# Kernel optimization log

Measured on AMD Instinct MI355X. Metric: run time of the kernel, lower is better.

## Reference

```python
import jax, jax.numpy as jnp
import numpy as np

B = 2; QD = 128; H = QD; W = QD; NQ = QD * QD
EMBED = 256; HEADS = 8; POINTS = 4; D = EMBED // HEADS; FFN = 512


def setup_inputs() -> dict:
    key = jax.random.key(0)
    ks = jax.random.split(key, 16)
    s = 0.02
    rn = lambda k, shp: jax.random.normal(k, shp, jnp.float32) * s
    return {
        'q': jax.random.normal(ks[0], (B, NQ, EMBED), jnp.float32),
        'W_off': rn(ks[1], (EMBED, HEADS * POINTS * 2)),
        'b_off': rn(ks[2], (HEADS * POINTS * 2,)),
        'W_attn': rn(ks[3], (EMBED, HEADS * POINTS)),
        'b_attn': rn(ks[4], (HEADS * POINTS,)),
        'W_val': rn(ks[5], (EMBED, EMBED)),
        'b_val': rn(ks[6], (EMBED,)),
        'W_out': rn(ks[7], (EMBED, EMBED)),
        'b_out': rn(ks[8], (EMBED,)),
        'W1': rn(ks[9], (EMBED, FFN)),
        'b1': rn(ks[10], (FFN,)),
        'W2': rn(ks[11], (FFN, EMBED)),
        'b2': rn(ks[12], (EMBED,)),
        'gamma': jnp.ones((EMBED,), jnp.float32),
        'beta': jnp.zeros((EMBED,), jnp.float32),
    }


def _layernorm(x, g, b):
    m = x.mean(-1, keepdims=True)
    v = ((x - m) ** 2).mean(-1, keepdims=True)
    return (x - m) * jax.lax.rsqrt(v + 1e-5) * g + b


def _msda(q, W_off, b_off, W_attn, b_attn, W_val, b_val, W_out, b_out):
    # value projection; value == query here. (B, NQ, EMBED)
    value = q @ W_val + b_val
    v = value.reshape(B, NQ, HEADS, D).transpose(0, 2, 1, 3)  # (B, heads, Nv, D)

    off = (q @ W_off + b_off).reshape(B, NQ, HEADS, POINTS, 2)
    aw = jax.nn.softmax((q @ W_attn + b_attn).reshape(B, NQ, HEADS, POINTS), axis=-1)

    # reference points: torch.meshgrid(linspace, linspace, indexing='xy')
    lin = jnp.linspace(0.0, 1.0, QD)
    gx, gy = jnp.meshgrid(lin, lin, indexing='xy')
    ref = jnp.stack([gx, gy], -1).reshape(1, NQ, 1, 1, 2)

    # offset_normalizer = [W, H]; sampling locations in [0,1]
    loc = ref + off / jnp.array([W, H], jnp.float32)
    # grid_sample bilinear, align_corners=False: pixel = loc * size - 0.5
    px = (loc[..., 0] * W - 0.5).transpose(0, 2, 1, 3)  # (B, heads, NQ, P)
    py = (loc[..., 1] * H - 0.5).transpose(0, 2, 1, 3)

    x0 = jnp.floor(px)
    y0 = jnp.floor(py)
    sampled = jnp.zeros((B, HEADS, NQ, POINTS, D), jnp.float32)
    for dy in (0.0, 1.0):
        for dx in (0.0, 1.0):
            xi = x0 + dx
            yi = y0 + dy
            wgt = (1.0 - jnp.abs(px - xi)) * (1.0 - jnp.abs(py - yi))
            valid = ((xi >= 0) & (xi <= W - 1) & (yi >= 0) & (yi <= H - 1)).astype(jnp.float32)
            idx = (jnp.clip(yi, 0, H - 1).astype(jnp.int32) * W
                   + jnp.clip(xi, 0, W - 1).astype(jnp.int32))  # (B, heads, NQ, P)
            g = jnp.take_along_axis(v, idx.reshape(B, HEADS, NQ * POINTS, 1), axis=2)
            g = g.reshape(B, HEADS, NQ, POINTS, D)
            sampled = sampled + g * (wgt * valid)[..., None]

    awt = aw.transpose(0, 2, 1, 3)  # (B, heads, NQ, P)
    out = (sampled * awt[..., None]).sum(3)  # (B, heads, NQ, D)
    out = out.transpose(0, 2, 1, 3).reshape(B, NQ, EMBED)
    # mmcv: dropout(output_proj(out)) + identity ; dropout is identity at eval
    return out @ W_out + b_out + q


def reference(q, W_off, b_off, W_attn, b_attn, W_val, b_val, W_out, b_out,
              W1, b1, W2, b2, gamma, beta):
    attn = _msda(q, W_off, b_off, W_attn, b_attn, W_val, b_val, W_out, b_out)
    x = attn + q  # outer residual in the module (in addition to mmcv's internal one)
    ffn = _layernorm(jax.nn.relu(x @ W1 + b1) @ W2 + b2, gamma, beta)
    return x + ffn
```

## Files before the change

kernel.cpp:

```cpp
#include <hip/hip_runtime.h>
#include <hip/hip_bf16.h>
#include <cstddef>
#include <cstdint>

#define B_      2
#define QD_     128
#define NQ_     (QD_ * QD_)
#define EMBED_  256
#define HEADS_  8
#define POINTS_ 4
#define FFN_    512
#define RTOT_   (B_ * NQ_)
#define NCATP_  384

using bf16x8 = __attribute__((ext_vector_type(8))) short;
using f32x4  = __attribute__((ext_vector_type(4))) float;

__device__ __forceinline__ short f2bf(float f) {
    unsigned u = __float_as_uint(f);
    u += 0x7FFFu + ((u >> 16) & 1u);
    return (short)(u >> 16);
}

#define WCAT_ELEMS  (NCATP_ * 256)
#define WOUT_ELEMS  (256 * 256)
#define W1_ELEMS    (512 * 256)
#define W2_ELEMS    (256 * 512)
#define PREP_TOTAL  (WCAT_ELEMS + WOUT_ELEMS + W1_ELEMS + W2_ELEMS)

__global__ __launch_bounds__(256) void prep_weights(
        const float* __restrict__ Wv, const float* __restrict__ Wo,
        const float* __restrict__ Wa, const float* __restrict__ bv,
        const float* __restrict__ bo, const float* __restrict__ ba,
        const float* __restrict__ W_out, const float* __restrict__ W1,
        const float* __restrict__ W2,
        short* __restrict__ WcatT, short* __restrict__ WoutT,
        short* __restrict__ W1T, short* __restrict__ W2T,
        float* __restrict__ bcat) {
    int idx = blockIdx.x * 256 + threadIdx.x;
    if (idx < WCAT_ELEMS) {
        int c = idx >> 8, k = idx & 255;
        float v = 0.f;
        if (c < 256)      v = Wv[k * 256 + c];
        else if (c < 320) v = Wo[k * 64 + (c - 256)];
        else if (c < 352) v = Wa[k * 32 + (c - 320)];
        WcatT[idx] = f2bf(v);
    } else if (idx < WCAT_ELEMS + WOUT_ELEMS) {
        int j = idx - WCAT_ELEMS; int c = j >> 8, k = j & 255;
        WoutT[j] = f2bf(W_out[k * 256 + c]);
    } else if (idx < WCAT_ELEMS + WOUT_ELEMS + W1_ELEMS) {
        int j = idx - (WCAT_ELEMS + WOUT_ELEMS); int c = j >> 8, k = j & 255;
        W1T[j] = f2bf(W1[k * 512 + c]);
    } else if (idx < PREP_TOTAL) {
        int j = idx - (WCAT_ELEMS + WOUT_ELEMS + W1_ELEMS); int c = j >> 9, k = j & 511;
        W2T[j] = f2bf(W2[k * 256 + c]);
    }
    if (idx < NCATP_) {
        float v = 0.f;
        if (idx < 256)      v = bv[idx];
        else if (idx < 320) v = bo[idx - 256];
        else if (idx < 352) v = ba[idx - 320];
        bcat[idx] = v;
    }
}

__global__ __launch_bounds__(256) void cvt_bf16(const float* __restrict__ in,
                                                short* __restrict__ out) {
    const size_t i = (size_t)blockIdx.x * 256 + threadIdx.x;
    const float4 f0 = *(const float4*)(in + i * 8);
    const float4 f1 = *(const float4*)(in + i * 8 + 4);
    bf16x8 v;
    v[0] = f2bf(f0.x); v[1] = f2bf(f0.y); v[2] = f2bf(f0.z); v[3] = f2bf(f0.w);
    v[4] = f2bf(f1.x); v[5] = f2bf(f1.y); v[6] = f2bf(f1.z); v[7] = f2bf(f1.w);
    *(bf16x8*)(out + i * 8) = v;
}

enum { EP_F32 = 0, EP_RELU_BF16 = 1, EP_ADD2Q_BOTH = 2, EP_SPLIT = 3 };

template <int EP>
__global__ __launch_bounds__(256) void gemm_mfma(
        const short* __restrict__ A,
        const short* __restrict__ Bt,
        const float* __restrict__ bias,
        const float* __restrict__ extra,
        float* __restrict__ Cf,
        short* __restrict__ Cb,
        int M, int N, int K) {
    __shared__ __align__(16) short As[128 * 64];
    __shared__ __align__(16) short Bs[128 * 64];

    const int t    = threadIdx.x;
    const int ln   = t & 63;
    const int w    = t >> 6;
    const int wr   = w >> 1;
    const int wc   = w & 1;
    const int lrow = ln & 15;
    const int lkg  = ln >> 4;
    const int row0 = blockIdx.y * 128;
    const int col0 = blockIdx.x * 128;

    f32x4 acc[4][4] = {};

    for (int k0 = 0; k0 < K; k0 += 64) {
        #pragma unroll
        for (int j = 0; j < 4; ++j) {
            const int c0 = (w * 4 + j) * 64;
            const int c  = c0 + ln;
            const int r  = c >> 3;
            const int s  = (c & 7) ^ (r & 7);
            const short* ga = A  + (size_t)(row0 + r) * K + (k0 + s * 8);
            const short* gb = Bt + (size_t)(col0 + r) * K + (k0 + s * 8);
            __builtin_amdgcn_global_load_lds(
                (const __attribute__((address_space(1))) void*)ga,
                (__attribute__((address_space(3))) void*)&As[c0 * 8], 16, 0, 0);
            __builtin_amdgcn_global_load_lds(
                (const __attribute__((address_space(1))) void*)gb,
                (__attribute__((address_space(3))) void*)&Bs[c0 * 8], 16, 0, 0);
        }
        __syncthreads();

        #pragma unroll
        for (int ks = 0; ks < 2; ++ks) {
            const int slot = ((ks * 4 + lkg) ^ (lrow & 7)) * 8;
            bf16x8 af[4], bfr[4];
            #pragma unroll
            for (int m = 0; m < 4; ++m)
                af[m] = *(const bf16x8*)&As[(wr * 64 + m * 16 + lrow) * 64 + slot];
            #pragma unroll
            for (int n = 0; n < 4; ++n)
                bfr[n] = *(const bf16x8*)&Bs[(wc * 64 + n * 16 + lrow) * 64 + slot];
            #pragma unroll
            for (int m = 0; m < 4; ++m)
                #pragma unroll
                for (int n = 0; n < 4; ++n)
                    acc[m][n] = __builtin_amdgcn_mfma_f32_16x16x32_bf16(
                        af[m], bfr[n], acc[m][n], 0, 0, 0);
        }
        __syncthreads();
    }

    const int orow = (ln >> 4) * 4;
    const int ocol = ln & 15;
    #pragma unroll
    for (int m = 0; m < 4; ++m) {
        #pragma unroll
        for (int n = 0; n < 4; ++n) {
            const int col = col0 + wc * 64 + n * 16 + ocol;
            const float bv = bias[col];
            #pragma unroll
            for (int rr = 0; rr < 4; ++rr) {
                const int row = row0 + wr * 64 + m * 16 + orow + rr;
                float v = acc[m][n][rr] + bv;
                if (EP == EP_SPLIT) {
                    if (col < 256) Cb[(size_t)row * 256 + col] = f2bf(v);
                    else           Cf[(size_t)row * 128 + (col - 256)] = v;
                } else if (EP == EP_RELU_BF16) {
                    Cb[(size_t)row * N + col] = f2bf(fmaxf(v, 0.f));
                } else if (EP == EP_ADD2Q_BOTH) {
                    v += 2.f * extra[(size_t)row * N + col];
                    Cf[(size_t)row * N + col] = v;
                    Cb[(size_t)row * N + col] = f2bf(v);
                } else {
                    Cf[(size_t)row * N + col] = v;
                }
            }
        }
    }
}

__global__ __launch_bounds__(256) void msda_sample(
        const float* __restrict__ pm, const short* __restrict__ vcomp,
        short* __restrict__ msda) {
    __shared__ int   s_off[8][32][4];
    __shared__ float s_c[8][32][4];

    const int t  = threadIdx.x;
    const int r0 = blockIdx.x * 8;
    const int bq = r0 >> 14;

    {
        const int g = t >> 5, cmb = t & 31, h = cmb >> 2, p = cmb & 3;
        const int r = r0 + g;
        const int n = r & (NQ_ - 1);
        const int gi = n >> 7, gj = n & 127;
        const float* pr = pm + (size_t)r * 128;

        const float l0 = pr[64 + h * 4 + 0], l1 = pr[64 + h * 4 + 1];
        const float l2 = pr[64 + h * 4 + 2], l3 = pr[64 + h * 4 + 3];
        const float mx = fmaxf(fmaxf(l0, l1), fmaxf(l2, l3));
        const float sum = expf(l0 - mx) + expf(l1 - mx) + expf(l2 - mx) + expf(l3 - mx);
        const float lp = pr[64 + h * 4 + p];
        const float aw = expf(lp - mx) / sum;

        const float ox = pr[h * 8 + p * 2 + 0];
        const float oy = pr[h * 8 + p * 2 + 1];
        const float px = (gj * (1.0f / 127.0f) + ox * (1.0f / 128.0f)) * 128.0f - 0.5f;
        const float py = (gi * (1.0f / 127.0f) + oy * (1.0f / 128.0f)) * 128.0f - 0.5f;
        const float x0f = floorf(px), y0f = floorf(py);
        const int   x0 = (int)x0f, y0 = (int)y0f;
        const float fx = px - x0f, fy = py - y0f;
        const int x0c = min(max(x0, 0), 127), x1c = min(max(x0 + 1, 0), 127);
        const int y0c = min(max(y0, 0), 127), y1c = min(max(y0 + 1, 0), 127);
        const float vx0 = ((unsigned)x0 <= 127u) ? 1.f : 0.f;
        const float vx1 = ((unsigned)(x0 + 1) <= 127u) ? 1.f : 0.f;
        const float vy0 = ((unsigned)y0 <= 127u) ? 1.f : 0.f;
        const float vy1 = ((unsigned)(y0 + 1) <= 127u) ? 1.f : 0.f;

        s_off[g][cmb][0] = (y0c * 128 + x0c) * 512;
        s_off[g][cmb][1] = (y0c * 128 + x1c) * 512;
        s_off[g][cmb][2] = (y1c * 128 + x0c) * 512;
        s_off[g][cmb][3] = (y1c * 128 + x1c) * 512;
        s_c[g][cmb][0] = aw * (1.f - fx) * (1.f - fy) * vx0 * vy0;
        s_c[g][cmb][1] = aw * fx * (1.f - fy) * vx1 * vy0;
        s_c[g][cmb][2] = aw * (1.f - fx) * fy * vx0 * vy1;
        s_c[g][cmb][3] = aw * fx * fy * vx1 * vy1;
    }
    __syncthreads();

    const int half = t >> 7;
    const int h    = (t >> 4) & 7;
    const int dd   = t & 15;
    const char* vb = (const char*)vcomp + ((size_t)bq * NQ_ * 256 + h * 32 + dd * 2) * 2;

    #pragma unroll
    for (int it = 0; it < 4; ++it) {
        const int g = it * 2 + half;
        float a0 = 0.f, a1 = 0.f;
        #pragma unroll
        for (int p = 0; p < 4; ++p) {
            const int cmb = h * 4 + p;
            #pragma unroll
            for (int k = 0; k < 4; ++k) {
                const unsigned u = *(const unsigned*)(vb + s_off[g][cmb][k]);
                const float c = s_c[g][cmb][k];
                a0 += c * __uint_as_float(u << 16);
                a1 += c * __uint_as_float(u & 0xffff0000u);
            }
        }
        const int r = r0 + g;
        const unsigned o = (unsigned)(unsigned short)f2bf(a0)
                         | ((unsigned)(unsigned short)f2bf(a1) << 16);
        *(unsigned*)&msda[(size_t)r * 256 + h * 32 + dd * 2] = o;
    }
}

__global__ __launch_bounds__(256) void ln_add(const float* __restrict__ y,
                                              const float* __restrict__ gamma,
                                              const float* __restrict__ beta,
                                              float* __restrict__ xout) {
    const int wave = threadIdx.x >> 6;
    const int lane = threadIdx.x & 63;
    const size_t row = (size_t)blockIdx.x * 4 + wave;

    const float4 yv = *(const float4*)(y + row * EMBED_ + lane * 4);
    float s  = yv.x + yv.y + yv.z + yv.w;
    float sq = yv.x * yv.x + yv.y * yv.y + yv.z * yv.z + yv.w * yv.w;
    #pragma unroll
    for (int o = 32; o; o >>= 1) {
        s  += __shfl_xor(s, o, 64);
        sq += __shfl_xor(sq, o, 64);
    }
    const float m   = s * (1.0f / EMBED_);
    const float var = sq * (1.0f / EMBED_) - m * m;
    const float rs  = rsqrtf(var + 1e-5f);

    const float4 xv = *(const float4*)(xout + row * EMBED_ + lane * 4);
    const float4 g  = *(const float4*)(gamma + lane * 4);
    const float4 bt = *(const float4*)(beta + lane * 4);
    float4 o4;
    o4.x = xv.x + (yv.x - m) * rs * g.x + bt.x;
    o4.y = xv.y + (yv.y - m) * rs * g.y + bt.y;
    o4.z = xv.z + (yv.z - m) * rs * g.z + bt.z;
    o4.w = xv.w + (yv.w - m) * rs * g.w + bt.w;
    *(float4*)(xout + row * EMBED_ + lane * 4) = o4;
}

extern "C" void kernel_launch(void* const* d_in, const int* in_sizes, int n_in,
                              void* d_out, int out_size, void* d_ws, size_t ws_size,
                              hipStream_t stream) {
    const float* q      = (const float*)d_in[0];
    const float* b_out  = (const float*)d_in[8];
    const float* b1     = (const float*)d_in[10];
    const float* b2     = (const float*)d_in[12];
    const float* gamma  = (const float*)d_in[13];
    const float* beta   = (const float*)d_in[14];

    float* x = (float*)d_out;

    char* w = (char*)d_ws;
    float* pm    = (float*)w;
    short* vcomp = (short*)(w + (size_t)RTOT_ * 128 * 4);
    float* ybuf  = (float*)w;
    w += (size_t)RTOT_ * 128 * 4 + (size_t)RTOT_ * 256 * 2;
    short* qbf  = (short*)w; w += (size_t)RTOT_ * EMBED_ * 2;
    short* msda = (short*)w; w += (size_t)RTOT_ * EMBED_ * 2;
    short* xbf  = (short*)w; w += (size_t)RTOT_ * EMBED_ * 2;
    short* hid  = (short*)w; w += (size_t)RTOT_ * FFN_ * 2;
    short* WcatT = (short*)w; w += WCAT_ELEMS * 2;
    short* WoutT = (short*)w; w += WOUT_ELEMS * 2;
    short* W1T   = (short*)w; w += W1_ELEMS * 2;
    short* W2T   = (short*)w; w += W2_ELEMS * 2;
    float* bcat  = (float*)w; w += NCATP_ * 4;

    prep_weights<<<(PREP_TOTAL + 255) / 256, 256, 0, stream>>>(
        q  == nullptr ? nullptr : (const float*)d_in[5],
        (const float*)d_in[1], (const float*)d_in[3],
        (const float*)d_in[6], (const float*)d_in[2], (const float*)d_in[4],
        (const float*)d_in[7], (const float*)d_in[9], (const float*)d_in[11],
        WcatT, WoutT, W1T, W2T, bcat);

    cvt_bf16<<<(RTOT_ * EMBED_ / 8 + 255) / 256, 256, 0, stream>>>(q, qbf);

    gemm_mfma<EP_SPLIT><<<dim3(NCATP_ / 128, RTOT_ / 128), 256, 0, stream>>>(
        qbf, WcatT, bcat, nullptr, pm, vcomp, RTOT_, NCATP_, EMBED_);

    msda_sample<<<RTOT_ / 8, 256, 0, stream>>>(pm, vcomp, msda);

    gemm_mfma<EP_ADD2Q_BOTH><<<dim3(EMBED_ / 128, RTOT_ / 128), 256, 0, stream>>>(
        msda, WoutT, b_out, q, x, xbf, RTOT_, EMBED_, EMBED_);

    gemm_mfma<EP_RELU_BF16><<<dim3(FFN_ / 128, RTOT_ / 128), 256, 0, stream>>>(
        xbf, W1T, b1, nullptr, nullptr, hid, RTOT_, FFN_, EMBED_);

    gemm_mfma<EP_F32><<<dim3(EMBED_ / 128, RTOT_ / 128), 256, 0, stream>>>(
        hid, W2T, b2, nullptr, ybuf, nullptr, RTOT_, EMBED_, FFN_);

    ln_add<<<RTOT_ / 4, 256, 0, stream>>>(ybuf, gamma, beta, x);
}
```

Before: 126.2 us.

## Fuse W2 GEMM with LayerNorm residual, use bf16 residuals, swizzle GEMM tiles

Replaces the final FFN GEMM plus separate LayerNorm kernel with a single gemm_ln kernel. Each block computes a full 64x256 row tile, does the row mean and variance reduction in shared memory and writes the final output, so the fp32 ybuf round-trip is gone. The residual x is now kept only in bf16: the out-projection epilogue reads q as bf16 and no longer writes an fp32 x, which cuts memory traffic at some cost in precision. It also adds an XCD-style block index swizzle in gemm_mfma to improve L2 locality.

```diff
diff --git a/kernel.cpp b/kernel.cpp
--- a/kernel.cpp
+++ b/kernel.cpp
@@ -20,6 +20,9 @@
     unsigned u = __float_as_uint(f);
     u += 0x7FFFu + ((u >> 16) & 1u);
     return (short)(u >> 16);
+}
+__device__ __forceinline__ float bf2f(short s) {
+    return __uint_as_float(((unsigned)(unsigned short)s) << 16);
 }
 
 #define WCAT_ELEMS  (NCATP_ * 256)
@@ -75,14 +78,14 @@
     *(bf16x8*)(out + i * 8) = v;
 }
 
-enum { EP_F32 = 0, EP_RELU_BF16 = 1, EP_ADD2Q_BOTH = 2, EP_SPLIT = 3 };
+enum { EP_RELU_BF16 = 1, EP_ADD2Q_BF16 = 2, EP_SPLIT = 3 };
 
 template <int EP>
 __global__ __launch_bounds__(256) void gemm_mfma(
         const short* __restrict__ A,
         const short* __restrict__ Bt,
         const float* __restrict__ bias,
-        const float* __restrict__ extra,
+        const short* __restrict__ extra,
         float* __restrict__ Cf,
         short* __restrict__ Cb,
         int M, int N, int K) {
@@ -96,8 +99,14 @@
     const int wc   = w & 1;
     const int lrow = ln & 15;
     const int lkg  = ln >> 4;
-    const int row0 = blockIdx.y * 128;
-    const int col0 = blockIdx.x * 128;
+
+    const int gx   = gridDim.x;
+    const int nwg  = gx * gridDim.y;
+    const int flat = blockIdx.y * gx + blockIdx.x;
+    const int q8   = nwg >> 3;
+    const int swz  = (flat & 7) * q8 + (flat >> 3);
+    const int row0 = (swz / gx) * 128;
+    const int col0 = (swz % gx) * 128;
 
     f32x4 acc[4][4] = {};
 
@@ -156,13 +165,134 @@
                     else           Cf[(size_t)row * 128 + (col - 256)] = v;
                 } else if (EP == EP_RELU_BF16) {
                     Cb[(size_t)row * N + col] = f2bf(fmaxf(v, 0.f));
-                } else if (EP == EP_ADD2Q_BOTH) {
-                    v += 2.f * extra[(size_t)row * N + col];
-                    Cf[(size_t)row * N + col] = v;
+                } else if (EP == EP_ADD2Q_BF16) {
+                    v += 2.f * bf2f(extra[(size_t)row * N + col]);
                     Cb[(size_t)row * N + col] = f2bf(v);
-                } else {
-                    Cf[(size_t)row * N + col] = v;
                 }
+            }
+        }
+    }
+}
+
+__global__ __launch_bounds__(256) void gemm_ln(
+        const short* __restrict__ A,
+        const short* __restrict__ Bt,
+        const float* __restrict__ bias,
+        const short* __restrict__ xres,
+        const float* __restrict__ gamma, const float* __restrict__ beta,
+        float* __restrict__ out, int M, int K) {
+    __shared__ __align__(16) short As[64 * 64];
+    __shared__ __align__(16) short Bs[256 * 64];
+    __shared__ float red[64][4][2];
+
+    const int t    = threadIdx.x;
+    const int ln   = t & 63;
+    const int w    = t >> 6;
+    const int lrow = ln & 15;
+    const int lkg  = ln >> 4;
+    const int row0 = blockIdx.x * 64;
+
+    f32x4 acc[4][4] = {};
+
+    for (int k0 = 0; k0 < K; k0 += 64) {
+        #pragma unroll
+        for (int j = 0; j < 2; ++j) {
+            const int c0 = (w * 2 + j) * 64;
+            const int c  = c0 + ln;
+            const int r  = c >> 3;
+            const int s  = (c & 7) ^ (r & 7);
+            const short* ga = A + (size_t)(row0 + r) * K + (k0 + s * 8);
+            __builtin_amdgcn_global_load_lds(
+                (const __attribute__((address_space(1))) void*)ga,
+                (__attribute__((address_space(3))) void*)&As[c0 * 8], 16, 0, 0);
+        }
+        #pragma unroll
+        for (int j = 0; j < 8; ++j) {
+            const int c0 = (w * 8 + j) * 64;
+            const int c  = c0 + ln;
+            const int r  = c >> 3;
+            const int s  = (c & 7) ^ (r & 7);
+            const short* gb = Bt + (size_t)r * K + (k0 + s * 8);
+            __builtin_amdgcn_global_load_lds(
+                (const __attribute__((address_space(1))) void*)gb,
+                (__attribute__((address_space(3))) void*)&Bs[c0 * 8], 16, 0, 0);
+        }
+        __syncthreads();
+
+        #pragma unroll
+        for (int ks = 0; ks < 2; ++ks) {
+            const int slot = ((ks * 4 + lkg) ^ (lrow & 7)) * 8;
+            bf16x8 af[4], bfr[4];
+            #pragma unroll
+            for (int m = 0; m < 4; ++m)
+                af[m] = *(const bf16x8*)&As[(m * 16 + lrow) * 64 + slot];
+            #pragma unroll
+            for (int n = 0; n < 4; ++n)
+                bfr[n] = *(const bf16x8*)&Bs[(w * 64 + n * 16 + lrow) * 64 + slot];
+            #pragma unroll
+            for (int m = 0; m < 4; ++m)
+                #pragma unroll
+                for (int n = 0; n < 4; ++n)
+                    acc[m][n] = __builtin_amdgcn_mfma_f32_16x16x32_bf16(
+                        af[m], bfr[n], acc[m][n], 0, 0, 0);
+        }
+        __syncthreads();
+    }
+
+    const int orow = (ln >> 4) * 4;
+    const int ocol = ln & 15;
+
+    #pragma unroll
+    for (int n = 0; n < 4; ++n) {
+        const float bv = bias[w * 64 + n * 16 + ocol];
+        #pragma unroll
+        for (int m = 0; m < 4; ++m)
+            #pragma unroll
+            for (int rr = 0; rr < 4; ++rr)
+                acc[m][n][rr] += bv;
+    }
+
+    #pragma unroll
+    for (int m = 0; m < 4; ++m) {
+        #pragma unroll
+        for (int rr = 0; rr < 4; ++rr) {
+            float s = 0.f, sq = 0.f;
+            #pragma unroll
+            for (int n = 0; n < 4; ++n) {
+                const float v = acc[m][n][rr];
+                s += v; sq += v * v;
+            }
+            #pragma unroll
+            for (int o = 1; o < 16; o <<= 1) {
+                s  += __shfl_xor(s, o, 64);
+                sq += __shfl_xor(sq, o, 64);
+            }
+            if (ocol == 0) {
+                const int row = m * 16 + orow + rr;
+                red[row][w][0] = s;
+                red[row][w][1] = sq;
+            }
+        }
+    }
+    __syncthreads();
+
+    #pragma unroll
+    for (int m = 0; m < 4; ++m) {
+        #pragma unroll
+        for (int rr = 0; rr < 4; ++rr) {
+            const int row = m * 16 + orow + rr;
+            float S  = red[row][0][0] + red[row][1][0] + red[row][2][0] + red[row][3][0];
+            float SQ = red[row][0][1] + red[row][1][1] + red[row][2][1] + red[row][3][1];
+            const float mean = S * (1.0f / 256.0f);
+            const float var  = SQ * (1.0f / 256.0f) - mean * mean;
+            const float rs   = rsqrtf(var + 1e-5f);
+            const size_t rbase = (size_t)(row0 + row) * 256;
+            #pragma unroll
+            for (int n = 0; n < 4; ++n) {
+                const int col = w * 64 + n * 16 + ocol;
+                const float o = bf2f(xres[rbase + col])
+                              + (acc[m][n][rr] - mean) * rs * gamma[col] + beta[col];
+                out[rbase + col] = o;
             }
         }
     }
@@ -244,37 +374,6 @@
     }
 }
 
-__global__ __launch_bounds__(256) void ln_add(const float* __restrict__ y,
-                                              const float* __restrict__ gamma,
-                                              const float* __restrict__ beta,
-                                              float* __restrict__ xout) {
-    const int wave = threadIdx.x >> 6;
-    const int lane = threadIdx.x & 63;
-    const size_t row = (size_t)blockIdx.x * 4 + wave;
-
-    const float4 yv = *(const float4*)(y + row * EMBED_ + lane * 4);
-    float s  = yv.x + yv.y + yv.z + yv.w;
-    float sq = yv.x * yv.x + yv.y * yv.y + yv.z * yv.z + yv.w * yv.w;
-    #pragma unroll
-    for (int o = 32; o; o >>= 1) {
-        s  += __shfl_xor(s, o, 64);
-        sq += __shfl_xor(sq, o, 64);
-    }
-    const float m   = s * (1.0f / EMBED_);
-    const float var = sq * (1.0f / EMBED_) - m * m;
-    const float rs  = rsqrtf(var + 1e-5f);
-
-    const float4 xv = *(const float4*)(xout + row * EMBED_ + lane * 4);
-    const float4 g  = *(const float4*)(gamma + lane * 4);
-    const float4 bt = *(const float4*)(beta + lane * 4);
-    float4 o4;
-    o4.x = xv.x + (yv.x - m) * rs * g.x + bt.x;
-    o4.y = xv.y + (yv.y - m) * rs * g.y + bt.y;
-    o4.z = xv.z + (yv.z - m) * rs * g.z + bt.z;
-    o4.w = xv.w + (yv.w - m) * rs * g.w + bt.w;
-    *(float4*)(xout + row * EMBED_ + lane * 4) = o4;
-}
-
 extern "C" void kernel_launch(void* const* d_in, const int* in_sizes, int n_in,
                               void* d_out, int out_size, void* d_ws, size_t ws_size,
                               hipStream_t stream) {
@@ -285,17 +384,15 @@
     const float* gamma  = (const float*)d_in[13];
     const float* beta   = (const float*)d_in[14];
 
-    float* x = (float*)d_out;
+    float* out = (float*)d_out;
 
     char* w = (char*)d_ws;
-    float* pm    = (float*)w;
-    short* vcomp = (short*)(w + (size_t)RTOT_ * 128 * 4);
-    float* ybuf  = (float*)w;
-    w += (size_t)RTOT_ * 128 * 4 + (size_t)RTOT_ * 256 * 2;
-    short* qbf  = (short*)w; w += (size_t)RTOT_ * EMBED_ * 2;
-    short* msda = (short*)w; w += (size_t)RTOT_ * EMBED_ * 2;
-    short* xbf  = (short*)w; w += (size_t)RTOT_ * EMBED_ * 2;
-    short* hid  = (short*)w; w += (size_t)RTOT_ * FFN_ * 2;
+    float* pm    = (float*)w; w += (size_t)RTOT_ * 128 * 4;
+    short* vcomp = (short*)w; w += (size_t)RTOT_ * 256 * 2;
+    short* qbf   = (short*)w; w += (size_t)RTOT_ * EMBED_ * 2;
+    short* msda  = (short*)w; w += (size_t)RTOT_ * EMBED_ * 2;
+    short* xbf   = (short*)w; w += (size_t)RTOT_ * EMBED_ * 2;
+    short* hid   = (short*)w; w += (size_t)RTOT_ * FFN_ * 2;
     short* WcatT = (short*)w; w += WCAT_ELEMS * 2;
     short* WoutT = (short*)w; w += WOUT_ELEMS * 2;
     short* W1T   = (short*)w; w += W1_ELEMS * 2;
@@ -303,8 +400,7 @@
     float* bcat  = (float*)w; w += NCATP_ * 4;
 
     prep_weights<<<(PREP_TOTAL + 255) / 256, 256, 0, stream>>>(
-        q  == nullptr ? nullptr : (const float*)d_in[5],
-        (const float*)d_in[1], (const float*)d_in[3],
+        (const float*)d_in[5], (const float*)d_in[1], (const float*)d_in[3],
         (const float*)d_in[6], (const float*)d_in[2], (const float*)d_in[4],
         (const float*)d_in[7], (const float*)d_in[9], (const float*)d_in[11],
         WcatT, WoutT, W1T, W2T, bcat);
@@ -316,14 +412,12 @@
 
     msda_sample<<<RTOT_ / 8, 256, 0, stream>>>(pm, vcomp, msda);
 
-    gemm_mfma<EP_ADD2Q_BOTH><<<dim3(EMBED_ / 128, RTOT_ / 128), 256, 0, stream>>>(
-        msda, WoutT, b_out, q, x, xbf, RTOT_, EMBED_, EMBED_);
+    gemm_mfma<EP_ADD2Q_BF16><<<dim3(EMBED_ / 128, RTOT_ / 128), 256, 0, stream>>>(
+        msda, WoutT, b_out, qbf, nullptr, xbf, RTOT_, EMBED_, EMBED_);
 
     gemm_mfma<EP_RELU_BF16><<<dim3(FFN_ / 128, RTOT_ / 128), 256, 0, stream>>>(
         xbf, W1T, b1, nullptr, nullptr, hid, RTOT_, FFN_, EMBED_);
 
-    gemm_mfma<EP_F32><<<dim3(EMBED_ / 128, RTOT_ / 128), 256, 0, stream>>>(
-        hid, W2T, b2, nullptr, ybuf, nullptr, RTOT_, EMBED_, FFN_);
-
-    ln_add<<<RTOT_ / 4, 256, 0, stream>>>(ybuf, gamma, beta, x);
-}
+    gemm_ln<<<RTOT_ / 64, 256, 0, stream>>>(
+        hid, W2T, b2, xbf, gamma, beta, out, RTOT_, FFN_);
+}
```

Measured after the change: 107.5 us. -14.9%, faster.
